# Kernel optimization log

Measured on AMD Instinct MI355X. Metric: run time of the kernel, lower is better.

## Reference

```python
import jax, jax.numpy as jnp
import numpy as np

T, H, E, F, K, FS = 2048, 2048, 64, 512, 8, 512


def setup_inputs() -> dict:
    key = jax.random.key(0)
    ks = jax.random.split(key, 6)
    s = 0.02
    return {
        "hidden_states": jax.random.normal(ks[0], (T, H), jnp.float32),
        # merged gate: E router logits + 1 shared-expert gate logit
        "W_gate": jax.random.normal(ks[1], (H, E + 1), jnp.float32) * s,
        # per-expert merged gate_up proj: [E, H, 2F]
        "W_gate_up": jax.random.normal(ks[2], (E, H, 2 * F), jnp.float32) * s,
        "W_down": jax.random.normal(ks[3], (E, F, H), jnp.float32) * s,
        # shared expert
        "Ws_gate_up": jax.random.normal(ks[4], (H, 2 * FS), jnp.float32) * s,
        "Ws_down": jax.random.normal(ks[5], (FS, H), jnp.float32) * s,
    }


def reference(hidden_states, W_gate, W_gate_up, W_down, Ws_gate_up, Ws_down):
    x = hidden_states  # [T, H]
    logits_all = x @ W_gate                      # [T, E+1]
    router_logits = logits_all[:, :E]
    shared_gate_logit = logits_all[:, E:]        # [T, 1]

    # FusedMoE routing: softmax -> top_k -> renormalize (norm_topk_prob=True)
    probs = jax.nn.softmax(router_logits.astype(jnp.float32), axis=-1)
    topk_w, topk_idx = jax.lax.top_k(probs, K)   # [T, K]
    topk_w = topk_w / jnp.sum(topk_w, axis=-1, keepdims=True)
    # dense combine weights [T, E] (zero for unselected experts)
    combine = jnp.zeros((T, E), probs.dtype).at[
        jnp.arange(T)[:, None], topk_idx].set(topk_w)

    # grouped expert GEMMs (dense reference: every expert sees all tokens,
    # combine-weights zero-out unrouted pairs)
    gu = jnp.einsum('th,ehf->etf', x, W_gate_up)   # [E, T, 2F]
    g, u = jnp.split(gu, 2, axis=-1)
    act = jax.nn.silu(g) * u                       # [E, T, F]
    # apply combine weight before down-proj to avoid [E, T, H] intermediate
    act = act * combine.T[:, :, None].astype(act.dtype)
    routed = jnp.einsum('etf,efh->th', act, W_down)  # [T, H]

    # shared expert (Qwen3NextMLP with sigmoid expert_gate)
    sgu = x @ Ws_gate_up                           # [T, 2FS]
    sg, su = jnp.split(sgu, 2, axis=-1)
    shared = (jax.nn.silu(sg) * su) @ Ws_down      # [T, H]
    shared = jax.nn.sigmoid(shared_gate_logit) * shared

    return shared + routed.astype(x.dtype)
```

## Files before the change

kernel.cpp:

```cpp
#include <hip/hip_runtime.h>
#include <hip/hip_bf16.h>
#include <math.h>

#define T_TOK 2048
#define H_DIM 2048
#define E_NUM 64
#define F_DIM 512
#define K_TOP 8
#define FS_DIM 512
#define NROWS (T_TOK * K_TOP)

typedef __attribute__((ext_vector_type(8))) short short8v;
typedef __attribute__((ext_vector_type(4))) float f32x4;

static __device__ __forceinline__ unsigned short f2bf(float f) {
    unsigned int u = __float_as_uint(f);
    u += 0x7fff + ((u >> 16) & 1);
    return (unsigned short)(u >> 16);
}

#define BCHUNK(row, k8) ((((k8) ^ ((row) + ((row) >> 3)))) & 7)
#define ASW32(r) (((r) >> 1) & 3)

typedef const unsigned int __attribute__((address_space(1))) gu32;
typedef unsigned int __attribute__((address_space(3))) lu32;
#define GLDS16(gsrc, ldst) \
    __builtin_amdgcn_global_load_lds((gu32*)(gsrc), (lu32*)(ldst), 16, 0, 0)

__global__ __launch_bounds__(256) void cvt_bf16_kernel(
    const float* __restrict__ in, unsigned short* __restrict__ out, int n8)
{
    int i = blockIdx.x * 256 + threadIdx.x;
    if (i < n8) {
        const float4* p = (const float4*)(in + (size_t)i * 8);
        float4 v0 = p[0], v1 = p[1];
        ushort4 a = make_ushort4(f2bf(v0.x), f2bf(v0.y), f2bf(v0.z), f2bf(v0.w));
        ushort4 b = make_ushort4(f2bf(v1.x), f2bf(v1.y), f2bf(v1.z), f2bf(v1.w));
        ushort4* q = (ushort4*)(out + (size_t)i * 8);
        q[0] = a; q[1] = b;
    }
}

__global__ __launch_bounds__(64) void router_kernel(
    const float* __restrict__ x, const float* __restrict__ Wg,
    int* __restrict__ topk_idx, float* __restrict__ topk_w,
    float* __restrict__ sgate, int* __restrict__ counts)
{
    const int t = blockIdx.x;
    const int lane = threadIdx.x;
    const float* xr = x + (size_t)t * H_DIM;

    float a0 = 0.f, a1 = 0.f, a2 = 0.f, a3 = 0.f;
    for (int h = 0; h < H_DIM; h += 4) {
        float4 xv = *(const float4*)&xr[h];
        a0 += xv.x * Wg[(h + 0) * 65 + lane];
        a1 += xv.y * Wg[(h + 1) * 65 + lane];
        a2 += xv.z * Wg[(h + 2) * 65 + lane];
        a3 += xv.w * Wg[(h + 3) * 65 + lane];
    }
    float logit = (a0 + a1) + (a2 + a3);

    float a64 = 0.f;
    for (int h = lane; h < H_DIM; h += 64) a64 += xr[h] * Wg[h * 65 + 64];
#pragma unroll
    for (int off = 32; off >= 1; off >>= 1) a64 += __shfl_xor(a64, off);

    float v = logit;
    float selv[K_TOP]; int seli[K_TOP];
#pragma unroll
    for (int k = 0; k < K_TOP; ++k) {
        float mv = v; int mi = lane;
#pragma unroll
        for (int off = 32; off >= 1; off >>= 1) {
            float ov = __shfl_xor(mv, off);
            int   oi = __shfl_xor(mi, off);
            if (ov > mv || (ov == mv && oi < mi)) { mv = ov; mi = oi; }
        }
        selv[k] = mv; seli[k] = mi;
        if (lane == mi) v = -INFINITY;
    }

    if (lane == 0) {
        float m = selv[0];
        float w[K_TOP]; float s = 0.f;
#pragma unroll
        for (int k = 0; k < K_TOP; ++k) { w[k] = __expf(selv[k] - m); s += w[k]; }
        float inv = 1.f / s;
#pragma unroll
        for (int k = 0; k < K_TOP; ++k) {
            topk_idx[t * K_TOP + k] = seli[k];
            topk_w[t * K_TOP + k] = w[k] * inv;
            atomicAdd(&counts[seli[k]], 1);
        }
        sgate[t] = 1.f / (1.f + __expf(-a64));
    }
}

__global__ __launch_bounds__(256) void bucket_kernel(
    const int* __restrict__ topk_idx, const float* __restrict__ topk_w,
    const int* __restrict__ counts, int* __restrict__ offsets,
    int* __restrict__ bucket_tok, float* __restrict__ bucket_w)
{
    const int e = blockIdx.x, thr = threadIdx.x;
    __shared__ int cnt[256];
    __shared__ int base_s;
    const int q0 = thr * 64;
    int c = 0;
    for (int q = 0; q < 64; ++q) c += (topk_idx[q0 + q] == e) ? 1 : 0;
    cnt[thr] = c;
    __syncthreads();
    if (thr == 0) {
        int off = 0;
        for (int i = 0; i < e; ++i) off += counts[i];
        offsets[e] = off;
        base_s = off;
        int run = 0;
        for (int i = 0; i < 256; ++i) { int tval = cnt[i]; cnt[i] = run; run += tval; }
    }
    __syncthreads();
    int pos = base_s + cnt[thr];
    for (int q = 0; q < 64; ++q) {
        int pp = q0 + q;
        if (topk_idx[pp] == e) {
            bucket_tok[pos] = pp >> 3;
            bucket_w[pos] = topk_w[pp];
            ++pos;
        }
    }
}

template<bool ROUTED>
__global__ __launch_bounds__(512, 6) void gu_mfma_kernel(
    const unsigned short* __restrict__ xb,
    const float* __restrict__ Wall,
    const int* __restrict__ counts, const int* __restrict__ offsets,
    const int* __restrict__ bucket_tok, const float* __restrict__ bucket_w,
    unsigned short* __restrict__ actout)
{
    constexpr int BM = 256;
    __shared__ __align__(16) unsigned short As[2][BM * 32];
    __shared__ __align__(16) unsigned short Bs[2][64 * 64];
    __shared__ int   toksS[BM];
    __shared__ float twsS[BM];

    const int tid  = threadIdx.x;
    const int lane = tid & 63;
    const int wid  = tid >> 6;
    const int wm = wid >> 1, wn = wid & 1;
    const int lrow = lane & 15, lhi = lane >> 4;

    int cblk, mt, ne, base;
    const float* W;
    if (ROUTED) {
        int nw = (blockIdx.x & 7) * ((int)gridDim.x >> 3) + (blockIdx.x >> 3);
        int e = nw >> 5; mt = (nw >> 4) & 1; cblk = nw & 15;
        ne = counts[e]; base = offsets[e];
        if (mt * BM >= ne) return;
        W = Wall + (size_t)e * H_DIM * (2 * F_DIM);
    } else {
        cblk = blockIdx.x; mt = blockIdx.y;
        ne = T_TOK; base = 0;
        W = Wall;
    }
    const int c0 = cblk * 32;

    const int n4 = (tid & 15) * 4;
    const int kb = (tid >> 4) * 2;
    const int n5 = n4 & 31;
    const int wcol = ((n5 < 16) ? 0 : (F_DIM - 16)) + c0 + (n4 >> 5) * 16 + n5;
    int wr_off[4];
#pragma unroll
    for (int cc = 0; cc < 4; ++cc) {
        int n = n4 + cc;
        wr_off[cc] = n * 64 + BCHUNK(n, kb >> 3) * 8 + (kb & 7);
    }
    const int rg = wn * 32 + lrow, ru = wn * 32 + 16 + lrow;
    int rdBg[2], rdBu[2];
#pragma unroll
    for (int ks = 0; ks < 2; ++ks) {
        int kc = ks * 4 + lhi;
        rdBg[ks] = rg * 64 + BCHUNK(rg, kc) * 8;
        rdBu[ks] = ru * 64 + BCHUNK(ru, kc) * 8;
    }
    int rdA[4];
#pragma unroll
    for (int fm = 0; fm < 4; ++fm) {
        int arow = wm * 64 + fm * 16 + lrow;
        rdA[fm] = arow * 32 + ((lhi ^ ASW32(arow)) << 3);
    }
    const int ar0 = wid * 32 + (lane >> 2);
    const int ar1 = ar0 + 16;
    const int NT   = H_DIM / 64;
    const int SMAX = H_DIM / 32;
    const int m0_stride = ROUTED ? (2 * BM) : ((int)gridDim.y * BM);

    for (int m0 = mt * BM; m0 < ne; m0 += m0_stride) {
        __syncthreads();
        if (tid < BM) {
            int idx = m0 + tid; bool v = idx < ne;
            if (ROUTED) {
                toksS[tid] = v ? bucket_tok[base + idx] : bucket_tok[base];
                twsS[tid]  = v ? bucket_w[base + idx] : 0.f;
            } else {
                toksS[tid] = v ? idx : (T_TOK - 1);
                twsS[tid]  = 1.f;
            }
        }
        __syncthreads();

        const int src0 = toksS[ar0] * H_DIM + (((lane & 3) ^ ASW32(ar0)) << 3);
        const int src1 = toksS[ar1] * H_DIM + (((lane & 3) ^ ASW32(ar1)) << 3);

        f32x4 acc[4][2];
#pragma unroll
        for (int i = 0; i < 4; ++i) {
            acc[i][0] = (f32x4){0.f, 0.f, 0.f, 0.f};
            acc[i][1] = (f32x4){0.f, 0.f, 0.f, 0.f};
        }

        float4 b0 = *(const float4*)&W[(size_t)kb * (2 * F_DIM) + wcol];
        float4 b1 = *(const float4*)&W[(size_t)(kb + 1) * (2 * F_DIM) + wcol];
        GLDS16(xb + src0, &As[0][(wid * 32) * 32]);
        GLDS16(xb + src1, &As[0][(wid * 32 + 16) * 32]);
#pragma unroll
        for (int cc = 0; cc < 4; ++cc)
            *(ushort2*)&Bs[0][wr_off[cc]] = make_ushort2(
                f2bf(((const float*)&b0)[cc]), f2bf(((const float*)&b1)[cc]));
        b0 = *(const float4*)&W[(size_t)(64 + kb) * (2 * F_DIM) + wcol];
        b1 = *(const float4*)&W[(size_t)(64 + kb + 1) * (2 * F_DIM) + wcol];
        __syncthreads();

        for (int s = 0; s < SMAX; ++s) {
            const int kt = s >> 1;
            if (s + 1 < SMAX) {
                const int kof = (s + 1) * 32;
                GLDS16(xb + src0 + kof, &As[(s + 1) & 1][(wid * 32) * 32]);
                GLDS16(xb + src1 + kof, &As[(s + 1) & 1][(wid * 32 + 16) * 32]);
            }
            if ((s & 1) && (kt + 1 < NT)) {
#pragma unroll
                for (int cc = 0; cc < 4; ++cc)
                    *(ushort2*)&Bs[(kt + 1) & 1][wr_off[cc]] = make_ushort2(
                        f2bf(((const float*)&b0)[cc]), f2bf(((const float*)&b1)[cc]));
                int knx = (kt + 2 < NT) ? (kt + 2) * 64 : (NT - 1) * 64;
                b0 = *(const float4*)&W[(size_t)(knx + kb) * (2 * F_DIM) + wcol];
                b1 = *(const float4*)&W[(size_t)(knx + kb + 1) * (2 * F_DIM) + wcol];
            }
            __builtin_amdgcn_sched_barrier(0);
            const unsigned short* A_ = As[s & 1];
            const unsigned short* B_ = Bs[kt & 1];
            const int ks = s & 1;
            short8v bg = *(const short8v*)&B_[rdBg[ks]];
            short8v bu = *(const short8v*)&B_[rdBu[ks]];
#pragma unroll
            for (int fm = 0; fm < 4; ++fm) {
                short8v af = *(const short8v*)&A_[rdA[fm]];
                acc[fm][0] = __builtin_amdgcn_mfma_f32_16x16x32_bf16(af, bg, acc[fm][0], 0, 0, 0);
                acc[fm][1] = __builtin_amdgcn_mfma_f32_16x16x32_bf16(af, bu, acc[fm][1], 0, 0, 0);
            }
            __syncthreads();
        }

        const int acol = c0 + wn * 16 + lrow;
#pragma unroll
        for (int fm = 0; fm < 4; ++fm) {
#pragma unroll
            for (int i = 0; i < 4; ++i) {
                int ml = wm * 64 + fm * 16 + lhi * 4 + i;
                int idx = m0 + ml;
                if (idx < ne) {
                    float gv = acc[fm][0][i], uv = acc[fm][1][i];
                    float s = gv / (1.f + __expf(-gv));
                    float val = s * uv * twsS[ml];
                    size_t orow = ROUTED ? (size_t)(base + idx) : (size_t)idx;
                    actout[orow * F_DIM + acol] = f2bf(val);
                }
            }
        }
    }
}

template<bool ROUTED>
__global__ __launch_bounds__(512, 6) void down_mfma_kernel(
    const unsigned short* __restrict__ actb,
    const float* __restrict__ Wall,
    const int* __restrict__ counts, const int* __restrict__ offsets,
    const int* __restrict__ bucket_tok, const float* __restrict__ sgate,
    float* __restrict__ out)
{
    constexpr int BM = 256;
    __shared__ __align__(16) unsigned short As[2][BM * 32];
    __shared__ __align__(16) unsigned short Bs[2][64 * 64];
    __shared__ int   toksS[BM];
    __shared__ float sgS[BM];

    const int tid  = threadIdx.x;
    const int lane = tid & 63;
    const int wid  = tid >> 6;
    const int wm = wid >> 1, wn = wid & 1;
    const int lrow = lane & 15, lhi = lane >> 4;

    int cblk, mt, ne, base;
    const float* W;
    if (ROUTED) {
        int nw = (blockIdx.x & 7) * ((int)gridDim.x >> 3) + (blockIdx.x >> 3);
        int e = nw >> 6; mt = (nw >> 5) & 1; cblk = nw & 31;
        ne = counts[e]; base = offsets[e];
        if (mt * BM >= ne) return;
        W = Wall + (size_t)e * F_DIM * H_DIM;
    } else {
        cblk = blockIdx.x; mt = blockIdx.y;
        ne = T_TOK; base = 0;
        W = Wall;
    }
    const int c0 = cblk * 64;

    const int n4 = (tid & 15) * 4;
    const int kb = (tid >> 4) * 2;
    const int wcol = c0 + n4;
    int wr_off[4];
#pragma unroll
    for (int cc = 0; cc < 4; ++cc) {
        int n = n4 + cc;
        wr_off[cc] = n * 64 + BCHUNK(n, kb >> 3) * 8 + (kb & 7);
    }
    const int r0 = wn * 32 + lrow, r1 = wn * 32 + 16 + lrow;
    int rdB0[2], rdB1[2];
#pragma unroll
    for (int ks = 0; ks < 2; ++ks) {
        int kc = ks * 4 + lhi;
        rdB0[ks] = r0 * 64 + BCHUNK(r0, kc) * 8;
        rdB1[ks] = r1 * 64 + BCHUNK(r1, kc) * 8;
    }
    int rdA[4];
#pragma unroll
    for (int fm = 0; fm < 4; ++fm) {
        int arow = wm * 64 + fm * 16 + lrow;
        rdA[fm] = arow * 32 + ((lhi ^ ASW32(arow)) << 3);
    }
    const int ar0 = wid * 32 + (lane >> 2);
    const int ar1 = ar0 + 16;
    const int NT   = F_DIM / 64;
    const int SMAX = F_DIM / 32;
    const int m0_stride = ROUTED ? (2 * BM) : ((int)gridDim.y * BM);

    for (int m0 = mt * BM; m0 < ne; m0 += m0_stride) {
        __syncthreads();
        if (tid < BM) {
            int idx = m0 + tid;
            if (ROUTED) {
                toksS[tid] = (idx < ne) ? bucket_tok[base + idx] : 0;
            } else {
                sgS[tid] = sgate[(idx < ne) ? idx : (T_TOK - 1)];
            }
        }
        __syncthreads();

        int g0 = ROUTED ? min(base + m0 + ar0, NROWS - 1) : min(m0 + ar0, T_TOK - 1);
        int g1 = ROUTED ? min(base + m0 + ar1, NROWS - 1) : min(m0 + ar1, T_TOK - 1);
        const int src0 = g0 * F_DIM + (((lane & 3) ^ ASW32(ar0)) << 3);
        const int src1 = g1 * F_DIM + (((lane & 3) ^ ASW32(ar1)) << 3);

        f32x4 acc[4][2];
#pragma unroll
        for (int i = 0; i < 4; ++i) {
            acc[i][0] = (f32x4){0.f, 0.f, 0.f, 0.f};
            acc[i][1] = (f32x4){0.f, 0.f, 0.f, 0.f};
        }

        float4 b0 = *(const float4*)&W[(size_t)kb * H_DIM + wcol];
        float4 b1 = *(const float4*)&W[(size_t)(kb + 1) * H_DIM + wcol];
        GLDS16(actb + src0, &As[0][(wid * 32) * 32]);
        GLDS16(actb + src1, &As[0][(wid * 32 + 16) * 32]);
#pragma unroll
        for (int cc = 0; cc < 4; ++cc)
            *(ushort2*)&Bs[0][wr_off[cc]] = make_ushort2(
                f2bf(((const float*)&b0)[cc]), f2bf(((const float*)&b1)[cc]));
        b0 = *(const float4*)&W[(size_t)(64 + kb) * H_DIM + wcol];
        b1 = *(const float4*)&W[(size_t)(64 + kb + 1) * H_DIM + wcol];
        __syncthreads();

        for (int s = 0; s < SMAX; ++s) {
            const int kt = s >> 1;
            if (s + 1 < SMAX) {
                const int kof = (s + 1) * 32;
                GLDS16(actb + src0 + kof, &As[(s + 1) & 1][(wid * 32) * 32]);
                GLDS16(actb + src1 + kof, &As[(s + 1) & 1][(wid * 32 + 16) * 32]);
            }
            if ((s & 1) && (kt + 1 < NT)) {
#pragma unroll
                for (int cc = 0; cc < 4; ++cc)
                    *(ushort2*)&Bs[(kt + 1) & 1][wr_off[cc]] = make_ushort2(
                        f2bf(((const float*)&b0)[cc]), f2bf(((const float*)&b1)[cc]));
                int knx = (kt + 2 < NT) ? (kt + 2) * 64 : (NT - 1) * 64;
                b0 = *(const float4*)&W[(size_t)(knx + kb) * H_DIM + wcol];
                b1 = *(const float4*)&W[(size_t)(knx + kb + 1) * H_DIM + wcol];
            }
            __builtin_amdgcn_sched_barrier(0);
            const unsigned short* A_ = As[s & 1];
            const unsigned short* B_ = Bs[kt & 1];
            const int ks = s & 1;
            short8v bf0 = *(const short8v*)&B_[rdB0[ks]];
            short8v bf1 = *(const short8v*)&B_[rdB1[ks]];
#pragma unroll
            for (int fm = 0; fm < 4; ++fm) {
                short8v af = *(const short8v*)&A_[rdA[fm]];
                acc[fm][0] = __builtin_amdgcn_mfma_f32_16x16x32_bf16(af, bf0, acc[fm][0], 0, 0, 0);
                acc[fm][1] = __builtin_amdgcn_mfma_f32_16x16x32_bf16(af, bf1, acc[fm][1], 0, 0, 0);
            }
            __syncthreads();
        }

#pragma unroll
        for (int fm = 0; fm < 4; ++fm) {
#pragma unroll
            for (int fn = 0; fn < 2; ++fn) {
                int col = c0 + wn * 32 + fn * 16 + lrow;
#pragma unroll
                for (int i = 0; i < 4; ++i) {
                    int ml = wm * 64 + fm * 16 + lhi * 4 + i;
                    int idx = m0 + ml;
                    if (idx < ne) {
                        if (ROUTED) {
                            atomicAdd(&out[(size_t)toksS[ml] * H_DIM + col], acc[fm][fn][i]);
                        } else {
                            out[(size_t)idx * H_DIM + col] = sgS[ml] * acc[fm][fn][i];
                        }
                    }
                }
            }
        }
    }
}

extern "C" void kernel_launch(void* const* d_in, const int* in_sizes, int n_in,
                              void* d_out, int out_size, void* d_ws, size_t ws_size,
                              hipStream_t stream) {
    const float* x    = (const float*)d_in[0];
    const float* Wg   = (const float*)d_in[1];
    const float* Wgu  = (const float*)d_in[2];
    const float* Wd   = (const float*)d_in[3];
    const float* Wsgu = (const float*)d_in[4];
    const float* Wsd  = (const float*)d_in[5];
    float* out = (float*)d_out;

    char* p = (char*)d_ws;
    auto alloc = [&](size_t bytes) {
        char* r = p;
        p += (bytes + 255) & ~(size_t)255;
        return r;
    };
    int*   topk_idx   = (int*)  alloc((size_t)T_TOK * K_TOP * sizeof(int));
    float* topk_w     = (float*)alloc((size_t)T_TOK * K_TOP * sizeof(float));
    float* sgate      = (float*)alloc((size_t)T_TOK * sizeof(float));
    int*   counts     = (int*)  alloc((size_t)E_NUM * sizeof(int));
    int*   offsets    = (int*)  alloc((size_t)E_NUM * sizeof(int));
    int*   bucket_tok = (int*)  alloc((size_t)NROWS * sizeof(int));
    float* bucket_w   = (float*)alloc((size_t)NROWS * sizeof(float));
    unsigned short* xb    = (unsigned short*)alloc((size_t)T_TOK * H_DIM * sizeof(short));
    unsigned short* act_r = (unsigned short*)alloc((size_t)NROWS * F_DIM * sizeof(short));
    unsigned short* act_s = (unsigned short*)alloc((size_t)T_TOK * FS_DIM * sizeof(short));

    hipMemsetAsync(counts, 0, E_NUM * sizeof(int), stream);
    cvt_bf16_kernel<<<(T_TOK * H_DIM / 8 + 255) / 256, 256, 0, stream>>>(x, xb, T_TOK * H_DIM / 8);
    router_kernel<<<T_TOK, 64, 0, stream>>>(x, Wg, topk_idx, topk_w, sgate, counts);
    bucket_kernel<<<E_NUM, 256, 0, stream>>>(topk_idx, topk_w, counts, offsets, bucket_tok, bucket_w);

    gu_mfma_kernel<true><<<16 * E_NUM * 2, 512, 0, stream>>>(
        xb, Wgu, counts, offsets, bucket_tok, bucket_w, act_r);
    gu_mfma_kernel<false><<<dim3(16, T_TOK / 256), 512, 0, stream>>>(
        xb, Wsgu, counts, offsets, bucket_tok, bucket_w, act_s);

    down_mfma_kernel<false><<<dim3(32, T_TOK / 256), 512, 0, stream>>>(
        act_s, Wsd, counts, offsets, bucket_tok, sgate, out);
    down_mfma_kernel<true><<<32 * E_NUM * 2, 512, 0, stream>>>(
        act_r, Wd, counts, offsets, bucket_tok, sgate, out);
}
```

Measured before the change: 745.4 us.

## Double N tile width in gate-up and down MoE MFMA kernels

Widens each block's output column tile from 64 to 128 in both the gate_up and down grouped GEMM kernels, so each wave computes a 4x4 grid of MFMA fragments instead of 4x2. This halves the number of blocks and halves how often each gathered token row of A is re-read across column blocks. The cost is more accumulator registers, twice the B shared-memory footprint, and a lower occupancy target (launch bounds 6 to 4). The weight staging is rewritten to load four K rows per thread and store them with ushort4 writes.

```diff
diff --git a/kernel.cpp b/kernel.cpp
--- a/kernel.cpp
+++ b/kernel.cpp
@@ -130,7 +130,7 @@
 }
 
 template<bool ROUTED>
-__global__ __launch_bounds__(512, 6) void gu_mfma_kernel(
+__global__ __launch_bounds__(512, 4) void gu_mfma_kernel(
     const unsigned short* __restrict__ xb,
     const float* __restrict__ Wall,
     const int* __restrict__ counts, const int* __restrict__ offsets,
@@ -139,7 +139,7 @@
 {
     constexpr int BM = 256;
     __shared__ __align__(16) unsigned short As[2][BM * 32];
-    __shared__ __align__(16) unsigned short Bs[2][64 * 64];
+    __shared__ __align__(16) unsigned short Bs[2][128 * 64];
     __shared__ int   toksS[BM];
     __shared__ float twsS[BM];
 
@@ -153,7 +153,7 @@
     const float* W;
     if (ROUTED) {
         int nw = (blockIdx.x & 7) * ((int)gridDim.x >> 3) + (blockIdx.x >> 3);
-        int e = nw >> 5; mt = (nw >> 4) & 1; cblk = nw & 15;
+        int e = nw >> 4; mt = (nw >> 3) & 1; cblk = nw & 7;
         ne = counts[e]; base = offsets[e];
         if (mt * BM >= ne) return;
         W = Wall + (size_t)e * H_DIM * (2 * F_DIM);
@@ -162,25 +162,27 @@
         ne = T_TOK; base = 0;
         W = Wall;
     }
-    const int c0 = cblk * 32;
-
-    const int n4 = (tid & 15) * 4;
-    const int kb = (tid >> 4) * 2;
-    const int n5 = n4 & 31;
-    const int wcol = ((n5 < 16) ? 0 : (F_DIM - 16)) + c0 + (n4 >> 5) * 16 + n5;
-    int wr_off[4];
+    const int c0 = cblk * 64;
+
+    const int n4 = (tid & 31) * 4;
+    const int kq = (tid >> 5) * 4;
+    const int grp = n4 >> 5;
+    const int srccol = c0 + (grp >> 1) * 32 + (n4 & 31) + ((grp & 1) ? F_DIM : 0);
+    int wrB[4];
 #pragma unroll
     for (int cc = 0; cc < 4; ++cc) {
         int n = n4 + cc;
-        wr_off[cc] = n * 64 + BCHUNK(n, kb >> 3) * 8 + (kb & 7);
-    }
-    const int rg = wn * 32 + lrow, ru = wn * 32 + 16 + lrow;
-    int rdBg[2], rdBu[2];
-#pragma unroll
-    for (int ks = 0; ks < 2; ++ks) {
-        int kc = ks * 4 + lhi;
-        rdBg[ks] = rg * 64 + BCHUNK(rg, kc) * 8;
-        rdBu[ks] = ru * 64 + BCHUNK(ru, kc) * 8;
+        wrB[cc] = n * 64 + BCHUNK(n, kq >> 3) * 8 + (kq & 7);
+    }
+    int rdB[4][2];
+#pragma unroll
+    for (int fn = 0; fn < 4; ++fn) {
+        int r = wn * 64 + fn * 16 + lrow;
+#pragma unroll
+        for (int ks = 0; ks < 2; ++ks) {
+            int kc = ks * 4 + lhi;
+            rdB[fn][ks] = r * 64 + BCHUNK(r, kc) * 8;
+        }
     }
     int rdA[4];
 #pragma unroll
@@ -211,23 +213,26 @@
         const int src0 = toksS[ar0] * H_DIM + (((lane & 3) ^ ASW32(ar0)) << 3);
         const int src1 = toksS[ar1] * H_DIM + (((lane & 3) ^ ASW32(ar1)) << 3);
 
-        f32x4 acc[4][2];
-#pragma unroll
-        for (int i = 0; i < 4; ++i) {
-            acc[i][0] = (f32x4){0.f, 0.f, 0.f, 0.f};
-            acc[i][1] = (f32x4){0.f, 0.f, 0.f, 0.f};
-        }
-
-        float4 b0 = *(const float4*)&W[(size_t)kb * (2 * F_DIM) + wcol];
-        float4 b1 = *(const float4*)&W[(size_t)(kb + 1) * (2 * F_DIM) + wcol];
+        f32x4 acc[4][4];
+#pragma unroll
+        for (int i = 0; i < 4; ++i)
+#pragma unroll
+            for (int j = 0; j < 4; ++j) acc[i][j] = (f32x4){0.f, 0.f, 0.f, 0.f};
+
+        float4 bq[4];
+#pragma unroll
+        for (int i = 0; i < 4; ++i)
+            bq[i] = *(const float4*)&W[(size_t)(kq + i) * (2 * F_DIM) + srccol];
         GLDS16(xb + src0, &As[0][(wid * 32) * 32]);
         GLDS16(xb + src1, &As[0][(wid * 32 + 16) * 32]);
 #pragma unroll
         for (int cc = 0; cc < 4; ++cc)
-            *(ushort2*)&Bs[0][wr_off[cc]] = make_ushort2(
-                f2bf(((const float*)&b0)[cc]), f2bf(((const float*)&b1)[cc]));
-        b0 = *(const float4*)&W[(size_t)(64 + kb) * (2 * F_DIM) + wcol];
-        b1 = *(const float4*)&W[(size_t)(64 + kb + 1) * (2 * F_DIM) + wcol];
+            *(ushort4*)&Bs[0][wrB[cc]] = make_ushort4(
+                f2bf(((const float*)&bq[0])[cc]), f2bf(((const float*)&bq[1])[cc]),
+                f2bf(((const float*)&bq[2])[cc]), f2bf(((const float*)&bq[3])[cc]));
+#pragma unroll
+        for (int i = 0; i < 4; ++i)
+            bq[i] = *(const float4*)&W[(size_t)(64 + kq + i) * (2 * F_DIM) + srccol];
         __syncthreads();
 
         for (int s = 0; s < SMAX; ++s) {
@@ -240,40 +245,47 @@
             if ((s & 1) && (kt + 1 < NT)) {
 #pragma unroll
                 for (int cc = 0; cc < 4; ++cc)
-                    *(ushort2*)&Bs[(kt + 1) & 1][wr_off[cc]] = make_ushort2(
-                        f2bf(((const float*)&b0)[cc]), f2bf(((const float*)&b1)[cc]));
+                    *(ushort4*)&Bs[(kt + 1) & 1][wrB[cc]] = make_ushort4(
+                        f2bf(((const float*)&bq[0])[cc]), f2bf(((const float*)&bq[1])[cc]),
+                        f2bf(((const float*)&bq[2])[cc]), f2bf(((const float*)&bq[3])[cc]));
                 int knx = (kt + 2 < NT) ? (kt + 2) * 64 : (NT - 1) * 64;
-                b0 = *(const float4*)&W[(size_t)(knx + kb) * (2 * F_DIM) + wcol];
-                b1 = *(const float4*)&W[(size_t)(knx + kb + 1) * (2 * F_DIM) + wcol];
+#pragma unroll
+                for (int i = 0; i < 4; ++i)
+                    bq[i] = *(const float4*)&W[(size_t)(knx + kq + i) * (2 * F_DIM) + srccol];
             }
             __builtin_amdgcn_sched_barrier(0);
             const unsigned short* A_ = As[s & 1];
             const unsigned short* B_ = Bs[kt & 1];
             const int ks = s & 1;
-            short8v bg = *(const short8v*)&B_[rdBg[ks]];
-            short8v bu = *(const short8v*)&B_[rdBu[ks]];
+            short8v bf[4];
+#pragma unroll
+            for (int fn = 0; fn < 4; ++fn) bf[fn] = *(const short8v*)&B_[rdB[fn][ks]];
 #pragma unroll
             for (int fm = 0; fm < 4; ++fm) {
                 short8v af = *(const short8v*)&A_[rdA[fm]];
-                acc[fm][0] = __builtin_amdgcn_mfma_f32_16x16x32_bf16(af, bg, acc[fm][0], 0, 0, 0);
-                acc[fm][1] = __builtin_amdgcn_mfma_f32_16x16x32_bf16(af, bu, acc[fm][1], 0, 0, 0);
+#pragma unroll
+                for (int fn = 0; fn < 4; ++fn)
+                    acc[fm][fn] = __builtin_amdgcn_mfma_f32_16x16x32_bf16(af, bf[fn], acc[fm][fn], 0, 0, 0);
             }
             __syncthreads();
         }
 
-        const int acol = c0 + wn * 16 + lrow;
 #pragma unroll
         for (int fm = 0; fm < 4; ++fm) {
 #pragma unroll
-            for (int i = 0; i < 4; ++i) {
-                int ml = wm * 64 + fm * 16 + lhi * 4 + i;
-                int idx = m0 + ml;
-                if (idx < ne) {
-                    float gv = acc[fm][0][i], uv = acc[fm][1][i];
-                    float s = gv / (1.f + __expf(-gv));
-                    float val = s * uv * twsS[ml];
-                    size_t orow = ROUTED ? (size_t)(base + idx) : (size_t)idx;
-                    actout[orow * F_DIM + acol] = f2bf(val);
+            for (int p = 0; p < 2; ++p) {
+                const int acol = c0 + wn * 32 + p * 16 + lrow;
+#pragma unroll
+                for (int i = 0; i < 4; ++i) {
+                    int ml = wm * 64 + fm * 16 + lhi * 4 + i;
+                    int idx = m0 + ml;
+                    if (idx < ne) {
+                        float gv = acc[fm][p][i], uv = acc[fm][p + 2][i];
+                        float sg = gv / (1.f + __expf(-gv));
+                        float val = sg * uv * twsS[ml];
+                        size_t orow = ROUTED ? (size_t)(base + idx) : (size_t)idx;
+                        actout[orow * F_DIM + acol] = f2bf(val);
+                    }
                 }
             }
         }
@@ -281,7 +293,7 @@
 }
 
 template<bool ROUTED>
-__global__ __launch_bounds__(512, 6) void down_mfma_kernel(
+__global__ __launch_bounds__(512, 4) void down_mfma_kernel(
     const unsigned short* __restrict__ actb,
     const float* __restrict__ Wall,
     const int* __restrict__ counts, const int* __restrict__ offsets,
@@ -290,7 +302,7 @@
 {
     constexpr int BM = 256;
     __shared__ __align__(16) unsigned short As[2][BM * 32];
-    __shared__ __align__(16) unsigned short Bs[2][64 * 64];
+    __shared__ __align__(16) unsigned short Bs[2][128 * 64];
     __shared__ int   toksS[BM];
     __shared__ float sgS[BM];
 
@@ -304,7 +316,7 @@
     const float* W;
     if (ROUTED) {
         int nw = (blockIdx.x & 7) * ((int)gridDim.x >> 3) + (blockIdx.x >> 3);
-        int e = nw >> 6; mt = (nw >> 5) & 1; cblk = nw & 31;
+        int e = nw >> 5; mt = (nw >> 4) & 1; cblk = nw & 15;
         ne = counts[e]; base = offsets[e];
         if (mt * BM >= ne) return;
         W = Wall + (size_t)e * F_DIM * H_DIM;
@@ -313,24 +325,26 @@
         ne = T_TOK; base = 0;
         W = Wall;
     }
-    const int c0 = cblk * 64;
-
-    const int n4 = (tid & 15) * 4;
-    const int kb = (tid >> 4) * 2;
-    const int wcol = c0 + n4;
-    int wr_off[4];
+    const int c0 = cblk * 128;
+
+    const int n4 = (tid & 31) * 4;
+    const int kq = (tid >> 5) * 4;
+    const int srccol = c0 + n4;
+    int wrB[4];
 #pragma unroll
     for (int cc = 0; cc < 4; ++cc) {
         int n = n4 + cc;
-        wr_off[cc] = n * 64 + BCHUNK(n, kb >> 3) * 8 + (kb & 7);
-    }
-    const int r0 = wn * 32 + lrow, r1 = wn * 32 + 16 + lrow;
-    int rdB0[2], rdB1[2];
-#pragma unroll
-    for (int ks = 0; ks < 2; ++ks) {
-        int kc = ks * 4 + lhi;
-        rdB0[ks] = r0 * 64 + BCHUNK(r0, kc) * 8;
-        rdB1[ks] = r1 * 64 + BCHUNK(r1, kc) * 8;
+        wrB[cc] = n * 64 + BCHUNK(n, kq >> 3) * 8 + (kq & 7);
+    }
+    int rdB[4][2];
+#pragma unroll
+    for (int fn = 0; fn < 4; ++fn) {
+        int r = wn * 64 + fn * 16 + lrow;
+#pragma unroll
+        for (int ks = 0; ks < 2; ++ks) {
+            int kc = ks * 4 + lhi;
+            rdB[fn][ks] = r * 64 + BCHUNK(r, kc) * 8;
+        }
     }
     int rdA[4];
 #pragma unroll
@@ -361,23 +375,26 @@
         const int src0 = g0 * F_DIM + (((lane & 3) ^ ASW32(ar0)) << 3);
         const int src1 = g1 * F_DIM + (((lane & 3) ^ ASW32(ar1)) << 3);
 
-        f32x4 acc[4][2];
-#pragma unroll
-        for (int i = 0; i < 4; ++i) {
-            acc[i][0] = (f32x4){0.f, 0.f, 0.f, 0.f};
-            acc[i][1] = (f32x4){0.f, 0.f, 0.f, 0.f};
-        }
-
-        float4 b0 = *(const float4*)&W[(size_t)kb * H_DIM + wcol];
-        float4 b1 = *(const float4*)&W[(size_t)(kb + 1) * H_DIM + wcol];
+        f32x4 acc[4][4];
+#pragma unroll
+        for (int i = 0; i < 4; ++i)
+#pragma unroll
+            for (int j = 0; j < 4; ++j) acc[i][j] = (f32x4){0.f, 0.f, 0.f, 0.f};
+
+        float4 bq[4];
+#pragma unroll
+        for (int i = 0; i < 4; ++i)
+            bq[i] = *(const float4*)&W[(size_t)(kq + i) * H_DIM + srccol];
         GLDS16(actb + src0, &As[0][(wid * 32) * 32]);
         GLDS16(actb + src1, &As[0][(wid * 32 + 16) * 32]);
 #pragma unroll
         for (int cc = 0; cc < 4; ++cc)
-            *(ushort2*)&Bs[0][wr_off[cc]] = make_ushort2(
-                f2bf(((const float*)&b0)[cc]), f2bf(((const float*)&b1)[cc]));
-        b0 = *(const float4*)&W[(size_t)(64 + kb) * H_DIM + wcol];
-        b1 = *(const float4*)&W[(size_t)(64 + kb + 1) * H_DIM + wcol];
+            *(ushort4*)&Bs[0][wrB[cc]] = make_ushort4(
+                f2bf(((const float*)&bq[0])[cc]), f2bf(((const float*)&bq[1])[cc]),
+                f2bf(((const float*)&bq[2])[cc]), f2bf(((const float*)&bq[3])[cc]));
+#pragma unroll
+        for (int i = 0; i < 4; ++i)
+            bq[i] = *(const float4*)&W[(size_t)(64 + kq + i) * H_DIM + srccol];
         __syncthreads();
 
         for (int s = 0; s < SMAX; ++s) {
@@ -390,23 +407,27 @@
             if ((s & 1) && (kt + 1 < NT)) {
 #pragma unroll
                 for (int cc = 0; cc < 4; ++cc)
-                    *(ushort2*)&Bs[(kt + 1) & 1][wr_off[cc]] = make_ushort2(
-                        f2bf(((const float*)&b0)[cc]), f2bf(((const float*)&b1)[cc]));
+                    *(ushort4*)&Bs[(kt + 1) & 1][wrB[cc]] = make_ushort4(
+                        f2bf(((const float*)&bq[0])[cc]), f2bf(((const float*)&bq[1])[cc]),
+                        f2bf(((const float*)&bq[2])[cc]), f2bf(((const float*)&bq[3])[cc]));
                 int knx = (kt + 2 < NT) ? (kt + 2) * 64 : (NT - 1) * 64;
-                b0 = *(const float4*)&W[(size_t)(knx + kb) * H_DIM + wcol];
-                b1 = *(const float4*)&W[(size_t)(knx + kb + 1) * H_DIM + wcol];
+#pragma unroll
+                for (int i = 0; i < 4; ++i)
+                    bq[i] = *(const float4*)&W[(size_t)(knx + kq + i) * H_DIM + srccol];
             }
             __builtin_amdgcn_sched_barrier(0);
             const unsigned short* A_ = As[s & 1];
             const unsigned short* B_ = Bs[kt & 1];
             const int ks = s & 1;
-            short8v bf0 = *(const short8v*)&B_[rdB0[ks]];
-            short8v bf1 = *(const short8v*)&B_[rdB1[ks]];
+            short8v bf[4];
+#pragma unroll
+            for (int fn = 0; fn < 4; ++fn) bf[fn] = *(const short8v*)&B_[rdB[fn][ks]];
 #pragma unroll
             for (int fm = 0; fm < 4; ++fm) {
                 short8v af = *(const short8v*)&A_[rdA[fm]];
-                acc[fm][0] = __builtin_amdgcn_mfma_f32_16x16x32_bf16(af, bf0, acc[fm][0], 0, 0, 0);
-                acc[fm][1] = __builtin_amdgcn_mfma_f32_16x16x32_bf16(af, bf1, acc[fm][1], 0, 0, 0);
+#pragma unroll
+                for (int fn = 0; fn < 4; ++fn)
+                    acc[fm][fn] = __builtin_amdgcn_mfma_f32_16x16x32_bf16(af, bf[fn], acc[fm][fn], 0, 0, 0);
             }
             __syncthreads();
         }
@@ -414,8 +435,8 @@
 #pragma unroll
         for (int fm = 0; fm < 4; ++fm) {
 #pragma unroll
-            for (int fn = 0; fn < 2; ++fn) {
-                int col = c0 + wn * 32 + fn * 16 + lrow;
+            for (int fn = 0; fn < 4; ++fn) {
+                int col = c0 + wn * 64 + fn * 16 + lrow;
 #pragma unroll
                 for (int i = 0; i < 4; ++i) {
                     int ml = wm * 64 + fm * 16 + lhi * 4 + i;
@@ -466,13 +487,13 @@
     router_kernel<<<T_TOK, 64, 0, stream>>>(x, Wg, topk_idx, topk_w, sgate, counts);
     bucket_kernel<<<E_NUM, 256, 0, stream>>>(topk_idx, topk_w, counts, offsets, bucket_tok, bucket_w);
 
-    gu_mfma_kernel<true><<<16 * E_NUM * 2, 512, 0, stream>>>(
+    gu_mfma_kernel<true><<<8 * E_NUM * 2, 512, 0, stream>>>(
         xb, Wgu, counts, offsets, bucket_tok, bucket_w, act_r);
-    gu_mfma_kernel<false><<<dim3(16, T_TOK / 256), 512, 0, stream>>>(
+    gu_mfma_kernel<false><<<dim3(8, T_TOK / 256), 512, 0, stream>>>(
         xb, Wsgu, counts, offsets, bucket_tok, bucket_w, act_s);
 
-    down_mfma_kernel<false><<<dim3(32, T_TOK / 256), 512, 0, stream>>>(
+    down_mfma_kernel<false><<<dim3(16, T_TOK / 256), 512, 0, stream>>>(
         act_s, Wsd, counts, offsets, bucket_tok, sgate, out);
-    down_mfma_kernel<true><<<32 * E_NUM * 2, 512, 0, stream>>>(
+    down_mfma_kernel<true><<<16 * E_NUM * 2, 512, 0, stream>>>(
         act_r, Wd, counts, offsets, bucket_tok, sgate, out);
 }
```

Result: no change. 741.4 us (-0.5%).
